# Kernel optimization log

Hardware: AMD Instinct MI355X
Metric: run time of the kernel (lower is better)

The kernel has to match this reference:

```python
import jax, jax.numpy as jnp
import numpy as np


def setup_inputs() -> dict:
    key = jax.random.key(0)
    ks = jax.random.split(key, 16)
    B, D, H = 65536, 64, 512
    s = 0.05
    inp = {
        "state": jax.random.normal(ks[0], (B, D), dtype=jnp.float32),
        "Wz0": jax.random.normal(ks[1], (H, D), dtype=jnp.float32) * s,
        "bz0": jax.random.normal(ks[2], (H,), dtype=jnp.float32) * s,
        "Wz1": jax.random.normal(ks[3], (H, H), dtype=jnp.float32) * s,
        "Wz2": jax.random.normal(ks[4], (H, H), dtype=jnp.float32) * s,
        "Wz3": jax.random.normal(ks[5], (H, H), dtype=jnp.float32) * s,
        "WzL": jax.random.normal(ks[6], (1, H), dtype=jnp.float32) * s,
        "Wx0": jax.random.normal(ks[7], (H, D), dtype=jnp.float32) * s,
        "bx0": jax.random.normal(ks[8], (H,), dtype=jnp.float32) * s,
        "Wx1": jax.random.normal(ks[9], (H, D), dtype=jnp.float32) * s,
        "bx1": jax.random.normal(ks[10], (H,), dtype=jnp.float32) * s,
        "Wx2": jax.random.normal(ks[11], (H, D), dtype=jnp.float32) * s,
        "bx2": jax.random.normal(ks[12], (H,), dtype=jnp.float32) * s,
        "WxL": jax.random.normal(ks[13], (1, D), dtype=jnp.float32) * s,
    }
    return inp


def reference(state, Wz0, bz0, Wz1, Wz2, Wz3, WzL, Wx0, bx0, Wx1, bx1, Wx2, bx2, WxL):
    sp = jax.nn.softplus

    def icnn_sum(x):  # x: [B, D] -> scalar (sum of per-sample convex outputs)
        z = sp(x @ Wz0.T + bz0)                      # [B, H]
        z = sp(z @ Wz1.T + x @ Wx0.T + bx0)          # [B, H]
        z = sp(z @ Wz2.T + x @ Wx1.T + bx1)          # [B, H]
        z = sp(z @ Wz3.T + x @ Wx2.T + bx2)          # [B, H]
        out = z @ WzL.T + x @ WxL.T                  # [B, 1]
        return out.sum()

    x = state - 1.0
    # Output is scalar per-sample, so grad of the batch-sum equals the stacked
    # per-sample jacobians computed by the torch Python loop.
    action = jax.grad(icnn_sum)(x)                   # [B, D]
    return action
```

## Files before the change

### kernel.cpp

```cpp
#include <hip/hip_runtime.h>

typedef unsigned short u16;
typedef unsigned int u32;
typedef unsigned long long u64;

#define B_TOTAL 65536
#define H 512
#define D 64
#define BM 64

typedef __bf16 bf16x8 __attribute__((ext_vector_type(8)));
typedef float f32x4 __attribute__((ext_vector_type(4)));

__device__ __forceinline__ u32 f2b(float f) {
  u32 u = __builtin_bit_cast(u32, f);
  return (u + 0x7fffu + ((u >> 16) & 1u)) >> 16;
}
__device__ __forceinline__ u16 f2bc(float f) {
  return __builtin_bit_cast(u16, (__bf16)f);
}
__device__ __forceinline__ float b2f(u32 bits) {
  return __builtin_bit_cast(float, bits << 16);
}

#define OFF_Wz0b 0
#define OFF_Wx0b 32768
#define OFF_Wx1b 65536
#define OFF_Wx2b 98304
#define OFF_Wz1b 131072
#define OFF_Wz2b 393216
#define OFF_Wz3b 655360
#define OFF_Wz1t 917504
#define OFF_Wz2t 1179648
#define OFF_Wz3t 1441792
#define OFF_Wz0t 1703936
#define OFF_Wx0t 1736704
#define OFF_Wx1t 1769472
#define OFF_Wx2t 1802240
#define OFF_WEND 1835008
#define WS_ELEMS OFF_WEND

__global__ __launch_bounds__(256) void prep_kernel(
    const float* __restrict__ Wz0, const float* __restrict__ Wz1,
    const float* __restrict__ Wz2, const float* __restrict__ Wz3,
    const float* __restrict__ Wx0, const float* __restrict__ Wx1,
    const float* __restrict__ Wx2, u16* __restrict__ wsb) {
  int i = blockIdx.x * 256 + threadIdx.x;
  const float* src;
  int NN, KK, trans, p;
  if (i < 131072) {
    int r = i >> 15; p = i & 32767;
    src = (r == 0) ? Wz0 : (r == 1) ? Wx0 : (r == 2) ? Wx1 : Wx2;
    NN = 512; KK = 64; trans = 0;
  } else if (i < 917504) {
    int j = i - 131072; int r = j >> 18; p = j & 262143;
    src = (r == 0) ? Wz1 : (r == 1) ? Wz2 : Wz3;
    NN = 512; KK = 512; trans = 0;
  } else if (i < 1703936) {
    int j = i - 917504; int r = j >> 18; p = j & 262143;
    src = (r == 0) ? Wz1 : (r == 1) ? Wz2 : Wz3;
    NN = 512; KK = 512; trans = 1;
  } else {
    int j = i - 1703936; int r = j >> 15; p = j & 32767;
    src = (r == 0) ? Wz0 : (r == 1) ? Wx0 : (r == 2) ? Wx1 : Wx2;
    NN = 64; KK = 512; trans = 1;
  }
  int jj = p & 7, lane = (p >> 3) & 63, blk = p >> 9;
  int kt_sh = (KK == 64) ? 1 : 4;
  int ntile = blk >> kt_sh;
  int kstep = blk & ((1 << kt_sh) - 1);
  int n = ntile * 16 + (lane & 15);
  int k = kstep * 32 + ((lane >> 4) << 3) + jj;
  float v = trans ? src[k * NN + n] : src[n * KK + k];
  wsb[i] = (u16)f2b(v);
}

__global__ __launch_bounds__(256) void fill_sentinel(float* out, int n) {
  int i = blockIdx.x * 256 + threadIdx.x;
  if (i < n) out[i] = 12345.0f;
}

__global__ __launch_bounds__(1024, 4) void icnn_kernel(
    const float* __restrict__ state,
    const float* __restrict__ bz0, const float* __restrict__ bx0,
    const float* __restrict__ bx1, const float* __restrict__ bx2,
    const float* __restrict__ WzL, const float* __restrict__ WxL,
    u16* __restrict__ wsw, float* __restrict__ out) {
  __shared__ u16 zbA[BM * H];
  __shared__ u16 zbB[BM * H];
  __shared__ u16 xbuf[BM * 72];

  const int tid = threadIdx.x;
  const int w = tid >> 6;
  const int lane = tid & 63;
  const int l15 = lane & 15;
  const int q = lane >> 4;
  const int blk = blockIdx.x;

  const u16* Wz0b = wsw + OFF_Wz0b;
  const u16* Wx0b = wsw + OFF_Wx0b;
  const u16* Wx1b = wsw + OFF_Wx1b;
  const u16* Wx2b = wsw + OFF_Wx2b;
  const u16* Wz1b = wsw + OFF_Wz1b;
  const u16* Wz2b = wsw + OFF_Wz2b;
  const u16* Wz3b = wsw + OFF_Wz3b;
  const u16* Wz1t = wsw + OFF_Wz1t;
  const u16* Wz2t = wsw + OFF_Wz2t;
  const u16* Wz3t = wsw + OFF_Wz3t;
  const u16* Wz0t = wsw + OFF_Wz0t;
  const u16* Wx0t = wsw + OFF_Wx0t;
  const u16* Wx1t = wsw + OFF_Wx1t;
  const u16* Wx2t = wsw + OFF_Wx2t;

  auto lbar = [&]() {
    asm volatile("s_waitcnt lgkmcnt(0)" ::: "memory");
    __builtin_amdgcn_s_barrier();
    asm volatile("" ::: "memory");
  };

  {
    int r = tid >> 4, c0 = (tid & 15) << 2;
    const float* p = state + (blk * BM + r) * D + c0;
    f32x4 v = __builtin_nontemporal_load((const f32x4*)p);
    u32* dst = (u32*)&xbuf[r * 72 + c0];
    dst[0] = (u32)f2bc(v[0] - 1.0f) | ((u32)f2bc(v[1] - 1.0f) << 16);
    dst[1] = (u32)f2bc(v[2] - 1.0f) | ((u32)f2bc(v[3] - 1.0f) << 16);
  }

  f32x4 acc[4][2];
  const f32x4 Z = {0.f, 0.f, 0.f, 0.f};
  f32x4 pk = Z;
  u64 sg0[8], sg1[8], sg2[8];

  auto ldA = [&](const u16* zb, int mt, int step) -> bf16x8 {
    return *(const bf16x8*)(&zb[(step * 4 + mt) * 512 + q * 128 + l15 * 8]);
  };
  auto ldX = [&](int mt, int ks) -> bf16x8 {
    return *(const bf16x8*)(&xbuf[(mt * 16 + l15) * 72 + ks * 32 + q * 8]);
  };
  auto wrZ = [&](u16* zb, int row, int n, u16 bits) {
    zb[((n >> 5) * 4 + (row >> 4)) * 512 + ((n >> 3) & 3) * 128 +
       (row & 15) * 8 + (n & 7)] = bits;
  };
  auto zeroAcc = [&]() {
#pragma unroll
    for (int mt = 0; mt < 4; ++mt)
#pragma unroll
      for (int nt = 0; nt < 2; ++nt) acc[mt][nt] = Z;
  };

  auto fwdX = [&](const u16* Wxp) {
    const u16* xb = Wxp + lane * 8;
#pragma unroll
    for (int ks = 0; ks < 2; ++ks) {
      bf16x8 b2[2];
#pragma unroll
      for (int nt = 0; nt < 2; ++nt)
        b2[nt] = *(const bf16x8*)(xb + ((w * 2 + nt) * 2 + ks) * 512);
#pragma unroll
      for (int mt = 0; mt < 4; ++mt) {
        bf16x8 ax = ldX(mt, ks);
#pragma unroll
        for (int nt = 0; nt < 2; ++nt) {
          f32x4 c = (ks == 0) ? Z : acc[mt][nt];
          acc[mt][nt] = __builtin_amdgcn_mfma_f32_16x16x32_bf16(ax, b2[nt], c, 0, 0, 0);
        }
      }
    }
  };

  auto fwdH = [&](const u16* Wp, const u16* zb) {
    const u16* gb = Wp + (w * 2 * 16) * 512 + lane * 8;
    bf16x8 bc0 = *(const bf16x8*)(gb);
    bf16x8 bc1 = *(const bf16x8*)(gb + 16 * 512);
#pragma unroll 2
    for (int st = 0; st < 16; ++st) {
      int stn = (st < 15) ? st + 1 : st;
      bf16x8 bn0 = *(const bf16x8*)(gb + stn * 512);
      bf16x8 bn1 = *(const bf16x8*)(gb + (16 + stn) * 512);
      bf16x8 a[4];
#pragma unroll
      for (int mt = 0; mt < 4; ++mt) a[mt] = ldA(zb, mt, st);
#pragma unroll
      for (int mt = 0; mt < 4; ++mt)
        acc[mt][0] = __builtin_amdgcn_mfma_f32_16x16x32_bf16(
            a[mt], bc0, acc[mt][0], 0, 0, 0);
#pragma unroll
      for (int mt = 0; mt < 4; ++mt)
        acc[mt][1] = __builtin_amdgcn_mfma_f32_16x16x32_bf16(
            a[mt], bc1, acc[mt][1], 0, 0, 0);
      bc0 = bn0; bc1 = bn1;
    }
  };

  auto fwd_epi = [&](const float* biasp, u64 (&sg)[8], u16* zb) {
    float bias[2];
#pragma unroll
    for (int nt = 0; nt < 2; ++nt) bias[nt] = biasp[(w * 2 + nt) * 16 + l15];
#pragma unroll
    for (int mt = 0; mt < 4; ++mt)
#pragma unroll
      for (int nt = 0; nt < 2; ++nt) {
        int n = (w * 2 + nt) * 16 + l15;
        f32x4 A = acc[mt][nt];
        u64 pack = 0;
#pragma unroll
        for (int r = 0; r < 4; ++r) {
          float a = A[r] + bias[nt];
          float t = __expf(-a);
          float u = 1.0f + t;
          float s = __builtin_amdgcn_rcpf(u);
          float z = a + __logf(u);
          pack |= (u64)f2bc(s) << (16 * r);
          wrZ(zb, mt * 16 + q * 4 + r, n, f2bc(z));
        }
        sg[mt * 2 + nt] = pack;
      }
  };
  auto d3_epi = [&](const float* biasp, u16* zb) {
    float bias[2], wl[2];
#pragma unroll
    for (int nt = 0; nt < 2; ++nt) {
      bias[nt] = biasp[(w * 2 + nt) * 16 + l15];
      wl[nt] = WzL[(w * 2 + nt) * 16 + l15];
    }
#pragma unroll
    for (int mt = 0; mt < 4; ++mt)
#pragma unroll
      for (int nt = 0; nt < 2; ++nt) {
        int n = (w * 2 + nt) * 16 + l15;
        f32x4 A = acc[mt][nt];
#pragma unroll
        for (int r = 0; r < 4; ++r) {
          float a = A[r] + bias[nt];
          float t = __expf(-a);
          float s = __builtin_amdgcn_rcpf(1.0f + t);
          wrZ(zb, mt * 16 + q * 4 + r, n, f2bc(wl[nt] * s));
        }
      }
  };
  auto bwd_epi = [&](const u64 (&sg)[8], u16* zb) {
#pragma unroll
    for (int mt = 0; mt < 4; ++mt)
#pragma unroll
      for (int nt = 0; nt < 2; ++nt) {
        int n = (w * 2 + nt) * 16 + l15;
        f32x4 A = acc[mt][nt];
        u64 v = sg[mt * 2 + nt];
#pragma unroll
        for (int r = 0; r < 4; ++r) {
          float s = b2f((u32)(v >> (16 * r)) & 0xffffu);
          wrZ(zb, mt * 16 + q * 4 + r, n, f2bc(A[r] * s));
        }
      }
  };

  auto minigrad = [&](const u16* Wg, const u16* zb, bool init) {
    int rt = w & 3, ct = w >> 2;
    const u16* gb = Wg + lane * 8;
    f32x4 t = init ? Z : pk;
#pragma unroll 4
    for (int st = 0; st < 16; ++st) {
      bf16x8 a = ldA(zb, rt, st);
      bf16x8 g = *(const bf16x8*)(gb + (ct * 16 + st) * 512);
      t = __builtin_amdgcn_mfma_f32_16x16x32_bf16(a, g, t, 0, 0, 0);
    }
    pk = t;
  };

  lbar();
  fwdX(Wz0b);
  fwd_epi(bz0, sg0, zbA);
  lbar();
  fwdX(Wx0b); fwdH(Wz1b, zbA);
  fwd_epi(bx0, sg1, zbB);
  lbar();
  fwdX(Wx1b); fwdH(Wz2b, zbB);
  fwd_epi(bx1, sg2, zbA);
  lbar();
  fwdX(Wx2b); fwdH(Wz3b, zbA);
  d3_epi(bx2, zbB);
  lbar();
  minigrad(Wx2t, zbB, true);
  zeroAcc(); fwdH(Wz3t, zbB);
  bwd_epi(sg2, zbA);
  lbar();
  minigrad(Wx1t, zbA, false);
  zeroAcc(); fwdH(Wz2t, zbA);
  bwd_epi(sg1, zbB);
  lbar();
  minigrad(Wx0t, zbB, false);
  zeroAcc(); fwdH(Wz1t, zbB);
  bwd_epi(sg0, zbA);
  lbar();
  minigrad(Wz0t, zbA, false);
  {
    int rt = w & 3, ct = w >> 2;
    float wx = WxL[ct * 16 + l15];
#pragma unroll
    for (int r = 0; r < 4; ++r) {
      int row = blk * BM + rt * 16 + q * 4 + r;
      out[row * D + ct * 16 + l15] = pk[r] + wx;
    }
  }
}

extern "C" void kernel_launch(void* const* d_in, const int* in_sizes, int n_in,
                              void* d_out, int out_size, void* d_ws, size_t ws_size,
                              hipStream_t stream) {
  const float* state = (const float*)d_in[0];
  const float* Wz0 = (const float*)d_in[1];
  const float* bz0 = (const float*)d_in[2];
  const float* Wz1 = (const float*)d_in[3];
  const float* Wz2 = (const float*)d_in[4];
  const float* Wz3 = (const float*)d_in[5];
  const float* WzL = (const float*)d_in[6];
  const float* Wx0 = (const float*)d_in[7];
  const float* bx0 = (const float*)d_in[8];
  const float* Wx1 = (const float*)d_in[9];
  const float* bx1 = (const float*)d_in[10];
  const float* Wx2 = (const float*)d_in[11];
  const float* bx2 = (const float*)d_in[12];
  const float* WxL = (const float*)d_in[13];

  if (ws_size < (size_t)WS_ELEMS * 2) {
    fill_sentinel<<<(out_size + 255) / 256, 256, 0, stream>>>((float*)d_out, out_size);
    return;
  }
  u16* wsw = (u16*)d_ws;
  prep_kernel<<<OFF_WEND / 256, 256, 0, stream>>>(Wz0, Wz1, Wz2, Wz3, Wx0, Wx1, Wx2, wsw);
  icnn_kernel<<<B_TOTAL / BM, 1024, 0, stream>>>(state, bz0, bx0, bx1, bx2, WzL, WxL,
                                                 wsw, (float*)d_out);
}
```

Before: 438.1 us.

## Switch to 32x32x16 MFMA tiles with padded LDS layout and split-K gradient reduction

Replaces the 16x16x32 bf16 MFMA tiling with 32x32x16 MFMAs. Each wave now owns a 64x32 output slab with two f32x16 accumulators. Weights are repacked into the matching fragment layout, and the activation buffers get a padded row stride (CH=520) to reduce LDS bank conflicts. The final input-gradient GEMM is split over K across 4 wave groups, with partial results parked in LDS and summed before output. This also adds s_setprio around the MFMA bursts. The aim is higher MFMA throughput and fewer LDS reads per flop, at the cost of an extra barrier and the reduction pass.

```diff
diff --git a/kernel.cpp b/kernel.cpp
--- a/kernel.cpp
+++ b/kernel.cpp
@@ -8,9 +8,11 @@
 #define H 512
 #define D 64
 #define BM 64
+#define CH 520
 
 typedef __bf16 bf16x8 __attribute__((ext_vector_type(8)));
 typedef float f32x4 __attribute__((ext_vector_type(4)));
+typedef float f32x16 __attribute__((ext_vector_type(16)));
 
 __device__ __forceinline__ u32 f2b(float f) {
   u32 u = __builtin_bit_cast(u32, f);
@@ -66,11 +68,11 @@
     NN = 64; KK = 512; trans = 1;
   }
   int jj = p & 7, lane = (p >> 3) & 63, blk = p >> 9;
-  int kt_sh = (KK == 64) ? 1 : 4;
+  int kt_sh = (KK == 64) ? 2 : 5;
   int ntile = blk >> kt_sh;
   int kstep = blk & ((1 << kt_sh) - 1);
-  int n = ntile * 16 + (lane & 15);
-  int k = kstep * 32 + ((lane >> 4) << 3) + jj;
+  int n = ntile * 32 + (lane & 31);
+  int k = kstep * 16 + ((lane >> 5) << 3) + jj;
   float v = trans ? src[k * NN + n] : src[n * KK + k];
   wsb[i] = (u16)f2b(v);
 }
@@ -86,15 +88,15 @@
     const float* __restrict__ bx1, const float* __restrict__ bx2,
     const float* __restrict__ WzL, const float* __restrict__ WxL,
     u16* __restrict__ wsw, float* __restrict__ out) {
-  __shared__ u16 zbA[BM * H];
-  __shared__ u16 zbB[BM * H];
+  __shared__ u16 zbA[64 * CH];
+  __shared__ u16 zbB[64 * CH];
   __shared__ u16 xbuf[BM * 72];
 
   const int tid = threadIdx.x;
   const int w = tid >> 6;
   const int lane = tid & 63;
-  const int l15 = lane & 15;
-  const int q = lane >> 4;
+  const int l31 = lane & 31;
+  const int q5 = lane >> 5;
   const int blk = blockIdx.x;
 
   const u16* Wz0b = wsw + OFF_Wz0b;
@@ -127,143 +129,113 @@
     dst[1] = (u32)f2bc(v[2] - 1.0f) | ((u32)f2bc(v[3] - 1.0f) << 16);
   }
 
-  f32x4 acc[4][2];
-  const f32x4 Z = {0.f, 0.f, 0.f, 0.f};
-  f32x4 pk = Z;
+  const f32x16 Z16 = {0,0,0,0,0,0,0,0,0,0,0,0,0,0,0,0};
+  f32x16 acc[2];
+  f32x16 pk = Z16;
   u64 sg0[8], sg1[8], sg2[8];
 
-  auto ldA = [&](const u16* zb, int mt, int step) -> bf16x8 {
-    return *(const bf16x8*)(&zb[(step * 4 + mt) * 512 + q * 128 + l15 * 8]);
-  };
-  auto ldX = [&](int mt, int ks) -> bf16x8 {
-    return *(const bf16x8*)(&xbuf[(mt * 16 + l15) * 72 + ks * 32 + q * 8]);
-  };
-  auto wrZ = [&](u16* zb, int row, int n, u16 bits) {
-    zb[((n >> 5) * 4 + (row >> 4)) * 512 + ((n >> 3) & 3) * 128 +
-       (row & 15) * 8 + (n & 7)] = bits;
-  };
-  auto zeroAcc = [&]() {
-#pragma unroll
-    for (int mt = 0; mt < 4; ++mt)
-#pragma unroll
-      for (int nt = 0; nt < 2; ++nt) acc[mt][nt] = Z;
+  auto ldA = [&](const u16* zb, int rt, int ks) -> bf16x8 {
+    return *(const bf16x8*)(&zb[(ks * 2 + rt) * CH + lane * 8]);
+  };
+  auto ldX = [&](int rt, int ks) -> bf16x8 {
+    return *(const bf16x8*)(&xbuf[(rt * 32 + l31) * 72 + ks * 16 + q5 * 8]);
   };
 
   auto fwdX = [&](const u16* Wxp) {
-    const u16* xb = Wxp + lane * 8;
-#pragma unroll
-    for (int ks = 0; ks < 2; ++ks) {
-      bf16x8 b2[2];
-#pragma unroll
-      for (int nt = 0; nt < 2; ++nt)
-        b2[nt] = *(const bf16x8*)(xb + ((w * 2 + nt) * 2 + ks) * 512);
-#pragma unroll
-      for (int mt = 0; mt < 4; ++mt) {
-        bf16x8 ax = ldX(mt, ks);
-#pragma unroll
-        for (int nt = 0; nt < 2; ++nt) {
-          f32x4 c = (ks == 0) ? Z : acc[mt][nt];
-          acc[mt][nt] = __builtin_amdgcn_mfma_f32_16x16x32_bf16(ax, b2[nt], c, 0, 0, 0);
-        }
-      }
+    const u16* xb = Wxp + (w * 4) * 512 + lane * 8;
+#pragma unroll
+    for (int ks = 0; ks < 4; ++ks) {
+      bf16x8 b = *(const bf16x8*)(xb + ks * 512);
+      bf16x8 a0 = ldX(0, ks);
+      bf16x8 a1 = ldX(1, ks);
+      acc[0] = __builtin_amdgcn_mfma_f32_32x32x16_bf16(a0, b, (ks == 0) ? Z16 : acc[0], 0, 0, 0);
+      acc[1] = __builtin_amdgcn_mfma_f32_32x32x16_bf16(a1, b, (ks == 0) ? Z16 : acc[1], 0, 0, 0);
     }
   };
 
   auto fwdH = [&](const u16* Wp, const u16* zb) {
-    const u16* gb = Wp + (w * 2 * 16) * 512 + lane * 8;
-    bf16x8 bc0 = *(const bf16x8*)(gb);
-    bf16x8 bc1 = *(const bf16x8*)(gb + 16 * 512);
+    const u16* gb = Wp + (w * 32) * 512 + lane * 8;
+    bf16x8 b0 = *(const bf16x8*)(gb);
+    bf16x8 b1 = *(const bf16x8*)(gb + 512);
 #pragma unroll 2
-    for (int st = 0; st < 16; ++st) {
-      int stn = (st < 15) ? st + 1 : st;
-      bf16x8 bn0 = *(const bf16x8*)(gb + stn * 512);
-      bf16x8 bn1 = *(const bf16x8*)(gb + (16 + stn) * 512);
-      bf16x8 a[4];
-#pragma unroll
-      for (int mt = 0; mt < 4; ++mt) a[mt] = ldA(zb, mt, st);
-#pragma unroll
-      for (int mt = 0; mt < 4; ++mt)
-        acc[mt][0] = __builtin_amdgcn_mfma_f32_16x16x32_bf16(
-            a[mt], bc0, acc[mt][0], 0, 0, 0);
-#pragma unroll
-      for (int mt = 0; mt < 4; ++mt)
-        acc[mt][1] = __builtin_amdgcn_mfma_f32_16x16x32_bf16(
-            a[mt], bc1, acc[mt][1], 0, 0, 0);
-      bc0 = bn0; bc1 = bn1;
+    for (int st = 0; st < 32; ++st) {
+      int stp = (st < 30) ? st + 2 : st;
+      bf16x8 bn = *(const bf16x8*)(gb + stp * 512);
+      bf16x8 a0 = ldA(zb, 0, st);
+      bf16x8 a1 = ldA(zb, 1, st);
+      __builtin_amdgcn_s_setprio(1);
+      acc[0] = __builtin_amdgcn_mfma_f32_32x32x16_bf16(a0, b0, acc[0], 0, 0, 0);
+      acc[1] = __builtin_amdgcn_mfma_f32_32x32x16_bf16(a1, b0, acc[1], 0, 0, 0);
+      __builtin_amdgcn_s_setprio(0);
+      b0 = b1; b1 = bn;
     }
   };
+  auto zeroAcc = [&]() { acc[0] = Z16; acc[1] = Z16; };
+
+  const int C0 = (2 * w + (l31 >> 4)) * (2 * CH) + ((l31 >> 3) & 1) * 256 + (l31 & 7);
 
   auto fwd_epi = [&](const float* biasp, u64 (&sg)[8], u16* zb) {
-    float bias[2];
-#pragma unroll
-    for (int nt = 0; nt < 2; ++nt) bias[nt] = biasp[(w * 2 + nt) * 16 + l15];
-#pragma unroll
-    for (int mt = 0; mt < 4; ++mt)
-#pragma unroll
-      for (int nt = 0; nt < 2; ++nt) {
-        int n = (w * 2 + nt) * 16 + l15;
-        f32x4 A = acc[mt][nt];
+    float bias = biasp[w * 32 + l31];
+#pragma unroll
+    for (int rt = 0; rt < 2; ++rt)
+#pragma unroll
+      for (int g = 0; g < 4; ++g) {
         u64 pack = 0;
 #pragma unroll
-        for (int r = 0; r < 4; ++r) {
-          float a = A[r] + bias[nt];
+        for (int e = 0; e < 4; ++e) {
+          float a = acc[rt][g * 4 + e] + bias;
           float t = __expf(-a);
           float u = 1.0f + t;
           float s = __builtin_amdgcn_rcpf(u);
           float z = a + __logf(u);
-          pack |= (u64)f2bc(s) << (16 * r);
-          wrZ(zb, mt * 16 + q * 4 + r, n, f2bc(z));
+          pack |= (u64)f2bc(s) << (16 * e);
+          zb[C0 + rt * CH + (e + 8 * g + 4 * q5) * 8] = f2bc(z);
         }
-        sg[mt * 2 + nt] = pack;
+        sg[rt * 4 + g] = pack;
       }
   };
   auto d3_epi = [&](const float* biasp, u16* zb) {
-    float bias[2], wl[2];
-#pragma unroll
-    for (int nt = 0; nt < 2; ++nt) {
-      bias[nt] = biasp[(w * 2 + nt) * 16 + l15];
-      wl[nt] = WzL[(w * 2 + nt) * 16 + l15];
-    }
-#pragma unroll
-    for (int mt = 0; mt < 4; ++mt)
-#pragma unroll
-      for (int nt = 0; nt < 2; ++nt) {
-        int n = (w * 2 + nt) * 16 + l15;
-        f32x4 A = acc[mt][nt];
-#pragma unroll
-        for (int r = 0; r < 4; ++r) {
-          float a = A[r] + bias[nt];
+    float bias = biasp[w * 32 + l31];
+    float wl = WzL[w * 32 + l31];
+#pragma unroll
+    for (int rt = 0; rt < 2; ++rt)
+#pragma unroll
+      for (int g = 0; g < 4; ++g)
+#pragma unroll
+        for (int e = 0; e < 4; ++e) {
+          float a = acc[rt][g * 4 + e] + bias;
           float t = __expf(-a);
           float s = __builtin_amdgcn_rcpf(1.0f + t);
-          wrZ(zb, mt * 16 + q * 4 + r, n, f2bc(wl[nt] * s));
+          zb[C0 + rt * CH + (e + 8 * g + 4 * q5) * 8] = f2bc(wl * s);
+        }
+  };
+  auto bwd_epi = [&](const u64 (&sg)[8], u16* zb) {
+#pragma unroll
+    for (int rt = 0; rt < 2; ++rt)
+#pragma unroll
+      for (int g = 0; g < 4; ++g) {
+        u64 v = sg[rt * 4 + g];
+#pragma unroll
+        for (int e = 0; e < 4; ++e) {
+          float s = b2f((u32)(v >> (16 * e)) & 0xffffu);
+          float d = acc[rt][g * 4 + e] * s;
+          zb[C0 + rt * CH + (e + 8 * g + 4 * q5) * 8] = f2bc(d);
         }
       }
   };
-  auto bwd_epi = [&](const u64 (&sg)[8], u16* zb) {
-#pragma unroll
-    for (int mt = 0; mt < 4; ++mt)
-#pragma unroll
-      for (int nt = 0; nt < 2; ++nt) {
-        int n = (w * 2 + nt) * 16 + l15;
-        f32x4 A = acc[mt][nt];
-        u64 v = sg[mt * 2 + nt];
-#pragma unroll
-        for (int r = 0; r < 4; ++r) {
-          float s = b2f((u32)(v >> (16 * r)) & 0xffffu);
-          wrZ(zb, mt * 16 + q * 4 + r, n, f2bc(A[r] * s));
-        }
-      }
-  };
 
   auto minigrad = [&](const u16* Wg, const u16* zb, bool init) {
-    int rt = w & 3, ct = w >> 2;
-    const u16* gb = Wg + lane * 8;
-    f32x4 t = init ? Z : pk;
-#pragma unroll 4
-    for (int st = 0; st < 16; ++st) {
-      bf16x8 a = ldA(zb, rt, st);
-      bf16x8 g = *(const bf16x8*)(gb + (ct * 16 + st) * 512);
-      t = __builtin_amdgcn_mfma_f32_16x16x32_bf16(a, g, t, 0, 0, 0);
+    int tr = w & 1, tc = (w >> 1) & 1, kq = w >> 2;
+    const u16* gb = Wg + (tc * 32 + kq * 8) * 512 + lane * 8;
+    f32x16 t = pk;
+    if (init) t = Z16;
+#pragma unroll 2
+    for (int i = 0; i < 8; ++i) {
+      bf16x8 a = ldA(zb, tr, kq * 8 + i);
+      bf16x8 g = *(const bf16x8*)(gb + i * 512);
+      __builtin_amdgcn_s_setprio(1);
+      t = __builtin_amdgcn_mfma_f32_32x32x16_bf16(a, g, t, 0, 0, 0);
+      __builtin_amdgcn_s_setprio(0);
     }
     pk = t;
   };
@@ -295,12 +267,27 @@
   lbar();
   minigrad(Wz0t, zbA, false);
   {
-    int rt = w & 3, ct = w >> 2;
-    float wx = WxL[ct * 16 + l15];
-#pragma unroll
-    for (int r = 0; r < 4; ++r) {
-      int row = blk * BM + rt * 16 + q * 4 + r;
-      out[row * D + ct * 16 + l15] = pk[r] + wx;
+    float* park = (float*)zbB;
+#pragma unroll
+    for (int reg = 0; reg < 16; ++reg)
+      park[(w * 16 + reg) * 64 + lane] = pk[reg];
+  }
+  lbar();
+  {
+    int t = w & 3, rg = w >> 2;
+    int tr = t & 1, tc = (t >> 1) & 1;
+    int col = tc * 32 + l31;
+    float wx = WxL[col];
+    const float* park = (const float*)zbB;
+#pragma unroll
+    for (int e = 0; e < 4; ++e) {
+      int reg = rg * 4 + e;
+      float v = park[(t * 16 + reg) * 64 + lane]
+              + park[((t + 4) * 16 + reg) * 64 + lane]
+              + park[((t + 8) * 16 + reg) * 64 + lane]
+              + park[((t + 12) * 16 + reg) * 64 + lane];
+      int row = blk * BM + tr * 32 + e + 8 * rg + 4 * q5;
+      out[row * D + col] = v + wx;
     }
   }
 }
```

New measurement: 414.0 us. 5.5% less time.
